# Optimization experiments

Hardware: AMD Instinct MI355X
Metric: run time of the kernel (lower is better)

The kernel has to match this reference:

```python
import jax, jax.numpy as jnp
import numpy as np

V, D, H, HD, T, B, L, BLK = 50257, 1024, 16, 64, 1024, 4, 6, 1024


def _ln_all(x):
    # F.layer_norm(x, (B, T, C)): normalize over the ENTIRE tensor, no affine
    mu = x.mean()
    var = ((x - mu) ** 2).mean()
    return (x - mu) * jax.lax.rsqrt(var + 1e-5)


def setup_inputs() -> dict:
    key = jax.random.key(0)
    ks = jax.random.split(key, 10)
    n = lambda k, shape, scale=1.0: jax.random.normal(k, shape, jnp.float32) * scale
    return {
        "idx": jax.random.randint(ks[0], (B, T), 0, V),
        "token_emb_table": n(ks[1], (V, D)),
        "position_emb_table": n(ks[2], (BLK, D)),
        "attention_q": n(ks[3], (D, H, HD), HD ** -0.5),
        "attention_k": n(ks[4], (D, H, HD), HD ** -0.5),
        "attention_v": n(ks[5], (D, H, HD), HD ** -0.5),
        "out_proj": n(ks[6], (H, HD, D), HD ** -0.5),
        "w_in": n(ks[7], (D, 4 * D), D ** -0.5),
        "w_out": n(ks[8], (4 * D, D), (4 * D) ** -0.5),
        "lm_head": n(ks[9], (D, V), D ** -0.5),
    }


def reference(idx, token_emb_table, position_emb_table, attention_q,
              attention_k, attention_v, out_proj, w_in, w_out, lm_head):
    Tt = idx.shape[1]
    x = token_emb_table[idx] + position_emb_table[:Tt]  # [B,T,D]
    mask = jnp.tril(jnp.ones((Tt, Tt), bool))
    scale = HD ** -0.5
    neg_inf = jnp.float32(-jnp.inf)
    # NOTE: the source shares ONE set of attention/MLP params across all layers.
    for _ in range(L):
        xn = _ln_all(x)
        q = jnp.einsum('btc,chd->bhtd', xn, attention_q)
        k = jnp.einsum('btc,chd->bhtd', xn, attention_k)
        v = jnp.einsum('btc,chd->bhtd', xn, attention_v)
        # verbatim (transposed-label) einsum from the source
        att = jnp.einsum('bhkd,bhqd->bhqk', q, k) * scale
        att = jnp.where(mask[None, None], att, neg_inf)
        att = jax.nn.softmax(att, axis=-1)
        out = jnp.einsum('bhqk,bhkd->bhqd', att, v)
        out = jnp.einsum('bhqd,hdc->bqc', out, out_proj)
        # dropout p=0 (eval) -> identity
        x = _ln_all(xn + out) + out
        # source bug: mlp_out = dropout(x) -> MLP (w_in/w_out) is dead code;
        # eval dropout is identity, so x = x + x
        x = x + x
    # forward returns x (post final full-tensor layernorm); lm_head unused w/o targets
    return _ln_all(x)
```

## Files before the change

### kernel.cpp

```cpp
#include <hip/hip_runtime.h>
#include <math.h>

#define TDIM 1024
#define DDIM 1024
#define NH   16
#define HDIM 64
#define BB   4
#define NLAYER 6
#define NTOK (BB*TDIM)
#define NELEM (NTOK*DDIM)

__global__ __launch_bounds__(256)
void k_embed(const int* __restrict__ idx, const float* __restrict__ tok,
             const float* __restrict__ pos, float* __restrict__ x) {
  int e4 = blockIdx.x * 256 + threadIdx.x;
  int e  = e4 * 4;
  int r  = e >> 10;
  int d  = e & 1023;
  int tp = r & (TDIM - 1);
  int id = idx[r];
  float4 a = *reinterpret_cast<const float4*>(&tok[(size_t)id * DDIM + d]);
  float4 p = *reinterpret_cast<const float4*>(&pos[(size_t)tp * DDIM + d]);
  float4 o = make_float4(a.x + p.x, a.y + p.y, a.z + p.z, a.w + p.w);
  reinterpret_cast<float4*>(x)[e4] = o;
}

__global__ __launch_bounds__(256)
void k_reduce1(const float* __restrict__ x, double* __restrict__ part) {
  int t = threadIdx.x;
  size_t base = (size_t)blockIdx.x * 1024;
  double s = 0.0, ss = 0.0;
  #pragma unroll
  for (int it = 0; it < 4; ++it) {
    double v = (double)x[base + it * 256 + t];
    s += v; ss += v * v;
  }
  __shared__ double rs[256], rq[256];
  rs[t] = s; rq[t] = ss; __syncthreads();
  for (int w = 128; w > 0; w >>= 1) {
    if (t < w) { rs[t] += rs[t + w]; rq[t] += rq[t + w]; }
    __syncthreads();
  }
  if (t == 0) { part[blockIdx.x * 2] = rs[0]; part[blockIdx.x * 2 + 1] = rq[0]; }
}

__global__ __launch_bounds__(1024)
void k_reduce2(const double* __restrict__ part, double* __restrict__ stats) {
  int t = threadIdx.x;
  double s = 0.0, ss = 0.0;
  #pragma unroll
  for (int it = 0; it < 4; ++it) {
    int p = it * 1024 + t;
    s  += part[p * 2];
    ss += part[p * 2 + 1];
  }
  __shared__ double rs[1024], rq[1024];
  rs[t] = s; rq[t] = ss; __syncthreads();
  for (int w = 512; w > 0; w >>= 1) {
    if (t < w) { rs[t] += rs[t + w]; rq[t] += rq[t + w]; }
    __syncthreads();
  }
  if (t == 0) {
    double mu  = rs[0] / (double)NELEM;
    double var = rq[0] / (double)NELEM - mu * mu;
    stats[0] = mu;
    stats[1] = 1.0 / sqrt(var + 1e-5);
  }
}

__global__ __launch_bounds__(256)
void k_norm4(const float* __restrict__ x, const double* __restrict__ stats,
             float* __restrict__ y) {
  int e4 = blockIdx.x * 256 + threadIdx.x;
  double mu = stats[0], rs = stats[1];
  float4 v = reinterpret_cast<const float4*>(x)[e4];
  float4 o = make_float4((float)(((double)v.x - mu) * rs),
                         (float)(((double)v.y - mu) * rs),
                         (float)(((double)v.z - mu) * rs),
                         (float)(((double)v.w - mu) * rs));
  reinterpret_cast<float4*>(y)[e4] = o;
}

__global__ __launch_bounds__(256)
void k_add4(float* __restrict__ t1, const float* __restrict__ proj) {
  int e4 = blockIdx.x * 256 + threadIdx.x;
  float4 a = reinterpret_cast<const float4*>(t1)[e4];
  float4 b = reinterpret_cast<const float4*>(proj)[e4];
  float4 o = make_float4(a.x + b.x, a.y + b.y, a.z + b.z, a.w + b.w);
  reinterpret_cast<float4*>(t1)[e4] = o;
}

__global__ __launch_bounds__(256)
void k_combine4(const float* __restrict__ t1, const float* __restrict__ proj,
                const double* __restrict__ stats, float* __restrict__ x) {
  int e4 = blockIdx.x * 256 + threadIdx.x;
  double mu = stats[0], rs = stats[1];
  float4 a = reinterpret_cast<const float4*>(t1)[e4];
  float4 b = reinterpret_cast<const float4*>(proj)[e4];
  float4 o = make_float4((float)(2.0 * (((double)a.x - mu) * rs + (double)b.x)),
                         (float)(2.0 * (((double)a.y - mu) * rs + (double)b.y)),
                         (float)(2.0 * (((double)a.z - mu) * rs + (double)b.z)),
                         (float)(2.0 * (((double)a.w - mu) * rs + (double)b.w)));
  reinterpret_cast<float4*>(x)[e4] = o;
}

__global__ __launch_bounds__(256)
void k_norm_out(const float* __restrict__ x, const double* __restrict__ stats,
                float* __restrict__ out) {
  int e4 = blockIdx.x * 256 + threadIdx.x;
  double mu = stats[0], rs = stats[1];
  float4 v = reinterpret_cast<const float4*>(x)[e4];
  float4 o = make_float4((float)(((double)v.x - mu) * rs),
                         (float)(((double)v.y - mu) * rs),
                         (float)(((double)v.z - mu) * rs),
                         (float)(((double)v.w - mu) * rs));
  reinterpret_cast<float4*>(out)[e4] = o;
}

__global__ __launch_bounds__(256)
void k_gemm(const float* __restrict__ A, const float* __restrict__ Bm,
            float* __restrict__ C, int scatter) {
  __shared__ float As[16][64];
  __shared__ float Bs[16][64];
  int t  = threadIdx.x;
  int m0 = blockIdx.y * 64;
  int n0 = blockIdx.x * 64;
  int tx = t & 15, ty = t >> 4;
  int ar = t >> 2;
  int ak = (t & 3) * 4;
  int br = t >> 4;
  int bc = (t & 15) * 4;
  double acc[4][4] = {};

  for (int kk = 0; kk < DDIM; kk += 16) {
    float4 av = *reinterpret_cast<const float4*>(&A[(size_t)(m0 + ar) * DDIM + kk + ak]);
    float4 bv = *reinterpret_cast<const float4*>(&Bm[(size_t)(kk + br) * DDIM + n0 + bc]);
    __syncthreads();
    As[ak + 0][ar] = av.x; As[ak + 1][ar] = av.y;
    As[ak + 2][ar] = av.z; As[ak + 3][ar] = av.w;
    Bs[br][bc + 0] = bv.x; Bs[br][bc + 1] = bv.y;
    Bs[br][bc + 2] = bv.z; Bs[br][bc + 3] = bv.w;
    __syncthreads();
    #pragma unroll
    for (int k = 0; k < 16; ++k) {
      float4 a4 = *reinterpret_cast<const float4*>(&As[k][ty * 4]);
      float4 b4 = *reinterpret_cast<const float4*>(&Bs[k][tx * 4]);
      double ad[4] = {(double)a4.x, (double)a4.y, (double)a4.z, (double)a4.w};
      double bd[4] = {(double)b4.x, (double)b4.y, (double)b4.z, (double)b4.w};
      #pragma unroll
      for (int i = 0; i < 4; ++i)
        #pragma unroll
        for (int j = 0; j < 4; ++j)
          acc[i][j] += ad[i] * bd[j];
    }
  }

  #pragma unroll
  for (int i = 0; i < 4; ++i) {
    int r  = m0 + ty * 4 + i;
    int b  = r >> 10;
    int tp = r & 1023;
    #pragma unroll
    for (int j = 0; j < 4; ++j) {
      int c = n0 + tx * 4 + j;
      float val = (float)acc[i][j];
      if (scatter) {
        int h = c >> 6, d = c & 63;
        C[((size_t)((b * NH + h) * TDIM + tp)) * HDIM + d] = val;
      } else {
        C[(size_t)r * DDIM + c] = val;
      }
    }
  }
}

__global__ __launch_bounds__(256)
void k_attn_flash(const float* __restrict__ q, const float* __restrict__ k,
                  const float* __restrict__ v, float* __restrict__ attout) {
  int it = blockIdx.x;
  int bh = blockIdx.y;
  int b  = bh >> 4, h = bh & 15;
  const float* qh = q + (size_t)bh * TDIM * HDIM;
  const float* kh = k + (size_t)bh * TDIM * HDIM;
  const float* vh = v + (size_t)bh * TDIM * HDIM;
  int i0 = it * 64;

  __shared__ float Ks[64][68];
  __shared__ float Qs[64][68];
  __shared__ float Vs[64][68];

  int t  = threadIdx.x;
  int tx = t & 15, ty = t >> 4;

  #pragma unroll
  for (int itr = 0; itr < 4; ++itr) {
    int f = t + 256 * itr;
    int r = f >> 4, dc = (f & 15) * 4;
    float4 val = *reinterpret_cast<const float4*>(&kh[(size_t)(i0 + r) * HDIM + dc]);
    Ks[dc + 0][r] = val.x; Ks[dc + 1][r] = val.y;
    Ks[dc + 2][r] = val.z; Ks[dc + 3][r] = val.w;
  }

  double O[4][4] = {};
  double m[4], l[4];
  #pragma unroll
  for (int i = 0; i < 4; ++i) { m[i] = -1.0e300; l[i] = 0.0; }

  for (int jt = 0; jt <= it; ++jt) {
    int j0 = jt * 64;

    float4 qv[4], vv[4];
    #pragma unroll
    for (int itr = 0; itr < 4; ++itr) {
      int f = t + 256 * itr;
      int r = f >> 4, dc = (f & 15) * 4;
      qv[itr] = *reinterpret_cast<const float4*>(&qh[(size_t)(j0 + r) * HDIM + dc]);
      vv[itr] = *reinterpret_cast<const float4*>(&vh[(size_t)(j0 + r) * HDIM + dc]);
    }
    __syncthreads();
    #pragma unroll
    for (int itr = 0; itr < 4; ++itr) {
      int f = t + 256 * itr;
      int r = f >> 4, dc = (f & 15) * 4;
      Qs[dc + 0][r] = qv[itr].x; Qs[dc + 1][r] = qv[itr].y;
      Qs[dc + 2][r] = qv[itr].z; Qs[dc + 3][r] = qv[itr].w;
      *reinterpret_cast<float4*>(&Vs[r][dc]) = vv[itr];
    }
    __syncthreads();

    double S[4][4] = {};
    #pragma unroll 16
    for (int d = 0; d < 64; ++d) {
      float4 kf = *reinterpret_cast<const float4*>(&Ks[d][ty * 4]);
      float4 qf = *reinterpret_cast<const float4*>(&Qs[d][tx * 4]);
      double kd[4] = {(double)kf.x, (double)kf.y, (double)kf.z, (double)kf.w};
      double qd[4] = {(double)qf.x, (double)qf.y, (double)qf.z, (double)qf.w};
      #pragma unroll
      for (int i = 0; i < 4; ++i)
        #pragma unroll
        for (int j = 0; j < 4; ++j)
          S[i][j] += kd[i] * qd[j];
    }

    double mloc[4];
    #pragma unroll
    for (int i = 0; i < 4; ++i) {
      #pragma unroll
      for (int j = 0; j < 4; ++j) {
        S[i][j] *= 0.125;
        if (jt == it && (tx * 4 + j) > (ty * 4 + i)) S[i][j] = -1.0e300;
      }
      mloc[i] = fmax(fmax(S[i][0], S[i][1]), fmax(S[i][2], S[i][3]));
    }
    #pragma unroll
    for (int xm = 1; xm < 16; xm <<= 1)
      #pragma unroll
      for (int i = 0; i < 4; ++i)
        mloc[i] = fmax(mloc[i], __shfl_xor(mloc[i], xm, 64));

    double p[4][4], tsum[4];
    #pragma unroll
    for (int i = 0; i < 4; ++i) {
      double mnew  = fmax(m[i], mloc[i]);
      double scale = exp(m[i] - mnew);
      m[i] = mnew;
      tsum[i] = 0.0;
      #pragma unroll
      for (int j = 0; j < 4; ++j) {
        p[i][j] = exp(S[i][j] - mnew);
        tsum[i] += p[i][j];
      }
      l[i] *= scale;
      #pragma unroll
      for (int j = 0; j < 4; ++j) O[i][j] *= scale;
    }
    #pragma unroll
    for (int xm = 1; xm < 16; xm <<= 1)
      #pragma unroll
      for (int i = 0; i < 4; ++i)
        tsum[i] += __shfl_xor(tsum[i], xm, 64);
    #pragma unroll
    for (int i = 0; i < 4; ++i) l[i] += tsum[i];

    __syncthreads();
    #pragma unroll
    for (int i = 0; i < 4; ++i)
      #pragma unroll
      for (int j = 0; j < 4; ++j)
        Qs[tx * 4 + j][ty * 4 + i] = (float)p[i][j];
    __syncthreads();

    #pragma unroll 16
    for (int jl = 0; jl < 64; ++jl) {
      float4 pf = *reinterpret_cast<const float4*>(&Qs[jl][ty * 4]);
      float4 vf = *reinterpret_cast<const float4*>(&Vs[jl][tx * 4]);
      double pd[4] = {(double)pf.x, (double)pf.y, (double)pf.z, (double)pf.w};
      double vd[4] = {(double)vf.x, (double)vf.y, (double)vf.z, (double)vf.w};
      #pragma unroll
      for (int i = 0; i < 4; ++i)
        #pragma unroll
        for (int j = 0; j < 4; ++j)
          O[i][j] += pd[i] * vd[j];
    }
  }

  #pragma unroll
  for (int i = 0; i < 4; ++i) {
    int ig = i0 + ty * 4 + i;
    double inv = 1.0 / l[i];
    float4 o;
    o.x = (float)(O[i][0] * inv); o.y = (float)(O[i][1] * inv);
    o.z = (float)(O[i][2] * inv); o.w = (float)(O[i][3] * inv);
    *reinterpret_cast<float4*>(
        &attout[((size_t)(b * TDIM + ig)) * DDIM + h * HDIM + tx * 4]) = o;
  }
}

extern "C" void kernel_launch(void* const* d_in, const int* in_sizes, int n_in,
                              void* d_out, int out_size, void* d_ws, size_t ws_size,
                              hipStream_t stream) {
  (void)in_sizes; (void)n_in; (void)out_size; (void)ws_size;
  const int*   idx = (const int*)d_in[0];
  const float* tok = (const float*)d_in[1];
  const float* pos = (const float*)d_in[2];
  const float* wq  = (const float*)d_in[3];
  const float* wk  = (const float*)d_in[4];
  const float* wv  = (const float*)d_in[5];
  const float* wo  = (const float*)d_in[6];
  float* out = (float*)d_out;

  float* ws   = (float*)d_ws;
  float* x    = ws;
  float* xn   = x   + NELEM;
  float* q    = xn  + NELEM;
  float* k    = q   + NELEM;
  float* v    = k   + NELEM;
  float* att  = x;
  float* proj = q;
  double* part  = (double*)(v + NELEM);
  double* stats = part + 8192;

  dim3 ggemm(DDIM / 64, NTOK / 64);
  dim3 gattn(TDIM / 64, BB * NH);

  k_embed<<<4096, 256, 0, stream>>>(idx, tok, pos, x);

  for (int l = 0; l < NLAYER; ++l) {
    k_reduce1<<<4096, 256, 0, stream>>>(x, part);
    k_reduce2<<<1, 1024, 0, stream>>>(part, stats);
    k_norm4<<<4096, 256, 0, stream>>>(x, stats, xn);
    k_gemm<<<ggemm, 256, 0, stream>>>(xn, wq, q, 1);
    k_gemm<<<ggemm, 256, 0, stream>>>(xn, wk, k, 1);
    k_gemm<<<ggemm, 256, 0, stream>>>(xn, wv, v, 1);
    k_attn_flash<<<gattn, 256, 0, stream>>>(q, k, v, att);
    k_gemm<<<ggemm, 256, 0, stream>>>(att, wo, proj, 0);
    k_add4<<<4096, 256, 0, stream>>>(xn, proj);
    k_reduce1<<<4096, 256, 0, stream>>>(xn, part);
    k_reduce2<<<1, 1024, 0, stream>>>(part, stats);
    k_combine4<<<4096, 256, 0, stream>>>(xn, proj, stats, x);
  }

  k_reduce1<<<4096, 256, 0, stream>>>(x, part);
  k_reduce2<<<1, 1024, 0, stream>>>(part, stats);
  k_norm_out<<<4096, 256, 0, stream>>>(x, stats, out);
}
```

Before: 9.107 ms.

## Store GEMM tiles as swizzled doubles with register prefetch; pair causal attention tiles

The GEMM now converts inputs to double once when writing shared memory, using padded and swizzled tiles. It prefetches the next global tile into registers while computing the current one, and writes outputs as float4. The attention kernel launches 8 blocks per head, each handling tile z and tile 15-z in turn, to balance causal work across blocks. This trades doubled shared memory and fewer, longer attention blocks for less per-FMA conversion and better load balance.

```diff
diff --git a/kernel.cpp b/kernel.cpp
--- a/kernel.cpp
+++ b/kernel.cpp
@@ -117,36 +117,49 @@
   reinterpret_cast<float4*>(out)[e4] = o;
 }
 
+#define SWZB(c) ((c) + ((c) >> 4))
 __global__ __launch_bounds__(256)
 void k_gemm(const float* __restrict__ A, const float* __restrict__ Bm,
             float* __restrict__ C, int scatter) {
-  __shared__ float As[16][64];
-  __shared__ float Bs[16][64];
+  __shared__ double As[16][68];
+  __shared__ double Bs[16][72];
   int t  = threadIdx.x;
   int m0 = blockIdx.y * 64;
   int n0 = blockIdx.x * 64;
   int tx = t & 15, ty = t >> 4;
-  int ar = t >> 2;
-  int ak = (t & 3) * 4;
-  int br = t >> 4;
-  int bc = (t & 15) * 4;
+  int ar = t >> 2, ak = (t & 3) * 4;
+  int br = t >> 4, bc = (t & 15) * 4;
+  int sb = SWZB(bc);
+
+  const float* Ap = &A[(size_t)(m0 + ar) * DDIM + ak];
+  const float* Bp = &Bm[(size_t)br * DDIM + n0 + bc];
+  float4 av = *reinterpret_cast<const float4*>(Ap);
+  float4 bv = *reinterpret_cast<const float4*>(Bp);
+
   double acc[4][4] = {};
+  int cA = ty * 4;
+  int cB = SWZB(tx * 4);
 
   for (int kk = 0; kk < DDIM; kk += 16) {
-    float4 av = *reinterpret_cast<const float4*>(&A[(size_t)(m0 + ar) * DDIM + kk + ak]);
-    float4 bv = *reinterpret_cast<const float4*>(&Bm[(size_t)(kk + br) * DDIM + n0 + bc]);
-    __syncthreads();
-    As[ak + 0][ar] = av.x; As[ak + 1][ar] = av.y;
-    As[ak + 2][ar] = av.z; As[ak + 3][ar] = av.w;
-    Bs[br][bc + 0] = bv.x; Bs[br][bc + 1] = bv.y;
-    Bs[br][bc + 2] = bv.z; Bs[br][bc + 3] = bv.w;
-    __syncthreads();
+    __syncthreads();
+    As[ak + 0][ar] = (double)av.x; As[ak + 1][ar] = (double)av.y;
+    As[ak + 2][ar] = (double)av.z; As[ak + 3][ar] = (double)av.w;
+    Bs[br][sb + 0] = (double)bv.x; Bs[br][sb + 1] = (double)bv.y;
+    Bs[br][sb + 2] = (double)bv.z; Bs[br][sb + 3] = (double)bv.w;
+    __syncthreads();
+
+    if (kk + 16 < DDIM) {
+      av = *reinterpret_cast<const float4*>(Ap + kk + 16);
+      bv = *reinterpret_cast<const float4*>(Bp + (size_t)(kk + 16) * DDIM);
+    }
+
     #pragma unroll
     for (int k = 0; k < 16; ++k) {
-      float4 a4 = *reinterpret_cast<const float4*>(&As[k][ty * 4]);
-      float4 b4 = *reinterpret_cast<const float4*>(&Bs[k][tx * 4]);
-      double ad[4] = {(double)a4.x, (double)a4.y, (double)a4.z, (double)a4.w};
-      double bd[4] = {(double)b4.x, (double)b4.y, (double)b4.z, (double)b4.w};
+      double ad[4], bd[4];
+      #pragma unroll
+      for (int i = 0; i < 4; ++i) ad[i] = As[k][cA + i];
+      #pragma unroll
+      for (int j = 0; j < 4; ++j) bd[j] = Bs[k][cB + j];
       #pragma unroll
       for (int i = 0; i < 4; ++i)
         #pragma unroll
@@ -160,16 +173,15 @@
     int r  = m0 + ty * 4 + i;
     int b  = r >> 10;
     int tp = r & 1023;
-    #pragma unroll
-    for (int j = 0; j < 4; ++j) {
-      int c = n0 + tx * 4 + j;
-      float val = (float)acc[i][j];
-      if (scatter) {
-        int h = c >> 6, d = c & 63;
-        C[((size_t)((b * NH + h) * TDIM + tp)) * HDIM + d] = val;
-      } else {
-        C[(size_t)r * DDIM + c] = val;
-      }
+    int cb = n0 + tx * 4;
+    float4 val = make_float4((float)acc[i][0], (float)acc[i][1],
+                             (float)acc[i][2], (float)acc[i][3]);
+    if (scatter) {
+      int h = cb >> 6, d = cb & 63;
+      *reinterpret_cast<float4*>(
+          &C[((size_t)((b * NH + h) * TDIM + tp)) * HDIM + d]) = val;
+    } else {
+      *reinterpret_cast<float4*>(&C[(size_t)r * DDIM + cb]) = val;
     }
   }
 }
@@ -177,13 +189,12 @@
 __global__ __launch_bounds__(256)
 void k_attn_flash(const float* __restrict__ q, const float* __restrict__ k,
                   const float* __restrict__ v, float* __restrict__ attout) {
-  int it = blockIdx.x;
+  int z  = blockIdx.x;
   int bh = blockIdx.y;
   int b  = bh >> 4, h = bh & 15;
   const float* qh = q + (size_t)bh * TDIM * HDIM;
   const float* kh = k + (size_t)bh * TDIM * HDIM;
   const float* vh = v + (size_t)bh * TDIM * HDIM;
-  int i0 = it * 64;
 
   __shared__ float Ks[64][68];
   __shared__ float Qs[64][68];
@@ -192,127 +203,134 @@
   int t  = threadIdx.x;
   int tx = t & 15, ty = t >> 4;
 
-  #pragma unroll
-  for (int itr = 0; itr < 4; ++itr) {
-    int f = t + 256 * itr;
-    int r = f >> 4, dc = (f & 15) * 4;
-    float4 val = *reinterpret_cast<const float4*>(&kh[(size_t)(i0 + r) * HDIM + dc]);
-    Ks[dc + 0][r] = val.x; Ks[dc + 1][r] = val.y;
-    Ks[dc + 2][r] = val.z; Ks[dc + 3][r] = val.w;
-  }
-
-  double O[4][4] = {};
-  double m[4], l[4];
-  #pragma unroll
-  for (int i = 0; i < 4; ++i) { m[i] = -1.0e300; l[i] = 0.0; }
-
-  for (int jt = 0; jt <= it; ++jt) {
-    int j0 = jt * 64;
-
-    float4 qv[4], vv[4];
+  for (int phase = 0; phase < 2; ++phase) {
+    int it = phase ? (15 - z) : z;
+    int i0 = it * 64;
+
+    __syncthreads();
+
     #pragma unroll
     for (int itr = 0; itr < 4; ++itr) {
       int f = t + 256 * itr;
       int r = f >> 4, dc = (f & 15) * 4;
-      qv[itr] = *reinterpret_cast<const float4*>(&qh[(size_t)(j0 + r) * HDIM + dc]);
-      vv[itr] = *reinterpret_cast<const float4*>(&vh[(size_t)(j0 + r) * HDIM + dc]);
-    }
-    __syncthreads();
+      float4 val = *reinterpret_cast<const float4*>(&kh[(size_t)(i0 + r) * HDIM + dc]);
+      Ks[dc + 0][r] = val.x; Ks[dc + 1][r] = val.y;
+      Ks[dc + 2][r] = val.z; Ks[dc + 3][r] = val.w;
+    }
+
+    double O[4][4] = {};
+    double m[4], l[4];
     #pragma unroll
-    for (int itr = 0; itr < 4; ++itr) {
-      int f = t + 256 * itr;
-      int r = f >> 4, dc = (f & 15) * 4;
-      Qs[dc + 0][r] = qv[itr].x; Qs[dc + 1][r] = qv[itr].y;
-      Qs[dc + 2][r] = qv[itr].z; Qs[dc + 3][r] = qv[itr].w;
-      *reinterpret_cast<float4*>(&Vs[r][dc]) = vv[itr];
-    }
-    __syncthreads();
-
-    double S[4][4] = {};
-    #pragma unroll 16
-    for (int d = 0; d < 64; ++d) {
-      float4 kf = *reinterpret_cast<const float4*>(&Ks[d][ty * 4]);
-      float4 qf = *reinterpret_cast<const float4*>(&Qs[d][tx * 4]);
-      double kd[4] = {(double)kf.x, (double)kf.y, (double)kf.z, (double)kf.w};
-      double qd[4] = {(double)qf.x, (double)qf.y, (double)qf.z, (double)qf.w};
+    for (int i = 0; i < 4; ++i) { m[i] = -1.0e300; l[i] = 0.0; }
+
+    for (int jt = 0; jt <= it; ++jt) {
+      int j0 = jt * 64;
+
+      float4 qv[4], vv[4];
+      #pragma unroll
+      for (int itr = 0; itr < 4; ++itr) {
+        int f = t + 256 * itr;
+        int r = f >> 4, dc = (f & 15) * 4;
+        qv[itr] = *reinterpret_cast<const float4*>(&qh[(size_t)(j0 + r) * HDIM + dc]);
+        vv[itr] = *reinterpret_cast<const float4*>(&vh[(size_t)(j0 + r) * HDIM + dc]);
+      }
+      __syncthreads();
+      #pragma unroll
+      for (int itr = 0; itr < 4; ++itr) {
+        int f = t + 256 * itr;
+        int r = f >> 4, dc = (f & 15) * 4;
+        Qs[dc + 0][r] = qv[itr].x; Qs[dc + 1][r] = qv[itr].y;
+        Qs[dc + 2][r] = qv[itr].z; Qs[dc + 3][r] = qv[itr].w;
+        *reinterpret_cast<float4*>(&Vs[r][dc]) = vv[itr];
+      }
+      __syncthreads();
+
+      double S[4][4] = {};
+      #pragma unroll 16
+      for (int d = 0; d < 64; ++d) {
+        float4 kf = *reinterpret_cast<const float4*>(&Ks[d][ty * 4]);
+        float4 qf = *reinterpret_cast<const float4*>(&Qs[d][tx * 4]);
+        double kd[4] = {(double)kf.x, (double)kf.y, (double)kf.z, (double)kf.w};
+        double qd[4] = {(double)qf.x, (double)qf.y, (double)qf.z, (double)qf.w};
+        #pragma unroll
+        for (int i = 0; i < 4; ++i)
+          #pragma unroll
+          for (int j = 0; j < 4; ++j)
+            S[i][j] += kd[i] * qd[j];
+      }
+
+      double mloc[4];
+      #pragma unroll
+      for (int i = 0; i < 4; ++i) {
+        #pragma unroll
+        for (int j = 0; j < 4; ++j) {
+          S[i][j] *= 0.125;
+          if (jt == it && (tx * 4 + j) > (ty * 4 + i)) S[i][j] = -1.0e300;
+        }
+        mloc[i] = fmax(fmax(S[i][0], S[i][1]), fmax(S[i][2], S[i][3]));
+      }
+      #pragma unroll
+      for (int xm = 1; xm < 16; xm <<= 1)
+        #pragma unroll
+        for (int i = 0; i < 4; ++i)
+          mloc[i] = fmax(mloc[i], __shfl_xor(mloc[i], xm, 64));
+
+      double p[4][4], tsum[4];
+      #pragma unroll
+      for (int i = 0; i < 4; ++i) {
+        double mnew  = fmax(m[i], mloc[i]);
+        double scale = exp(m[i] - mnew);
+        m[i] = mnew;
+        tsum[i] = 0.0;
+        #pragma unroll
+        for (int j = 0; j < 4; ++j) {
+          p[i][j] = exp(S[i][j] - mnew);
+          tsum[i] += p[i][j];
+        }
+        l[i] *= scale;
+        #pragma unroll
+        for (int j = 0; j < 4; ++j) O[i][j] *= scale;
+      }
+      #pragma unroll
+      for (int xm = 1; xm < 16; xm <<= 1)
+        #pragma unroll
+        for (int i = 0; i < 4; ++i)
+          tsum[i] += __shfl_xor(tsum[i], xm, 64);
+      #pragma unroll
+      for (int i = 0; i < 4; ++i) l[i] += tsum[i];
+
+      __syncthreads();
       #pragma unroll
       for (int i = 0; i < 4; ++i)
         #pragma unroll
         for (int j = 0; j < 4; ++j)
-          S[i][j] += kd[i] * qd[j];
-    }
-
-    double mloc[4];
+          Qs[tx * 4 + j][ty * 4 + i] = (float)p[i][j];
+      __syncthreads();
+
+      #pragma unroll 16
+      for (int jl = 0; jl < 64; ++jl) {
+        float4 pf = *reinterpret_cast<const float4*>(&Qs[jl][ty * 4]);
+        float4 vf = *reinterpret_cast<const float4*>(&Vs[jl][tx * 4]);
+        double pd[4] = {(double)pf.x, (double)pf.y, (double)pf.z, (double)pf.w};
+        double vd[4] = {(double)vf.x, (double)vf.y, (double)vf.z, (double)vf.w};
+        #pragma unroll
+        for (int i = 0; i < 4; ++i)
+          #pragma unroll
+          for (int j = 0; j < 4; ++j)
+            O[i][j] += pd[i] * vd[j];
+      }
+    }
+
     #pragma unroll
     for (int i = 0; i < 4; ++i) {
-      #pragma unroll
-      for (int j = 0; j < 4; ++j) {
-        S[i][j] *= 0.125;
-        if (jt == it && (tx * 4 + j) > (ty * 4 + i)) S[i][j] = -1.0e300;
-      }
-      mloc[i] = fmax(fmax(S[i][0], S[i][1]), fmax(S[i][2], S[i][3]));
-    }
-    #pragma unroll
-    for (int xm = 1; xm < 16; xm <<= 1)
-      #pragma unroll
-      for (int i = 0; i < 4; ++i)
-        mloc[i] = fmax(mloc[i], __shfl_xor(mloc[i], xm, 64));
-
-    double p[4][4], tsum[4];
-    #pragma unroll
-    for (int i = 0; i < 4; ++i) {
-      double mnew  = fmax(m[i], mloc[i]);
-      double scale = exp(m[i] - mnew);
-      m[i] = mnew;
-      tsum[i] = 0.0;
-      #pragma unroll
-      for (int j = 0; j < 4; ++j) {
-        p[i][j] = exp(S[i][j] - mnew);
-        tsum[i] += p[i][j];
-      }
-      l[i] *= scale;
-      #pragma unroll
-      for (int j = 0; j < 4; ++j) O[i][j] *= scale;
-    }
-    #pragma unroll
-    for (int xm = 1; xm < 16; xm <<= 1)
-      #pragma unroll
-      for (int i = 0; i < 4; ++i)
-        tsum[i] += __shfl_xor(tsum[i], xm, 64);
-    #pragma unroll
-    for (int i = 0; i < 4; ++i) l[i] += tsum[i];
-
-    __syncthreads();
-    #pragma unroll
-    for (int i = 0; i < 4; ++i)
-      #pragma unroll
-      for (int j = 0; j < 4; ++j)
-        Qs[tx * 4 + j][ty * 4 + i] = (float)p[i][j];
-    __syncthreads();
-
-    #pragma unroll 16
-    for (int jl = 0; jl < 64; ++jl) {
-      float4 pf = *reinterpret_cast<const float4*>(&Qs[jl][ty * 4]);
-      float4 vf = *reinterpret_cast<const float4*>(&Vs[jl][tx * 4]);
-      double pd[4] = {(double)pf.x, (double)pf.y, (double)pf.z, (double)pf.w};
-      double vd[4] = {(double)vf.x, (double)vf.y, (double)vf.z, (double)vf.w};
-      #pragma unroll
-      for (int i = 0; i < 4; ++i)
-        #pragma unroll
-        for (int j = 0; j < 4; ++j)
-          O[i][j] += pd[i] * vd[j];
-    }
-  }
-
-  #pragma unroll
-  for (int i = 0; i < 4; ++i) {
-    int ig = i0 + ty * 4 + i;
-    double inv = 1.0 / l[i];
-    float4 o;
-    o.x = (float)(O[i][0] * inv); o.y = (float)(O[i][1] * inv);
-    o.z = (float)(O[i][2] * inv); o.w = (float)(O[i][3] * inv);
-    *reinterpret_cast<float4*>(
-        &attout[((size_t)(b * TDIM + ig)) * DDIM + h * HDIM + tx * 4]) = o;
+      int ig = i0 + ty * 4 + i;
+      double inv = 1.0 / l[i];
+      float4 o;
+      o.x = (float)(O[i][0] * inv); o.y = (float)(O[i][1] * inv);
+      o.z = (float)(O[i][2] * inv); o.w = (float)(O[i][3] * inv);
+      *reinterpret_cast<float4*>(
+          &attout[((size_t)(b * TDIM + ig)) * DDIM + h * HDIM + tx * 4]) = o;
+    }
   }
 }
 
@@ -341,7 +359,7 @@
   double* stats = part + 8192;
 
   dim3 ggemm(DDIM / 64, NTOK / 64);
-  dim3 gattn(TDIM / 64, BB * NH);
+  dim3 gattn(8, BB * NH);
 
   k_embed<<<4096, 256, 0, stream>>>(idx, tok, pos, x);
 
```

After: 7.896 ms. -13.3%, faster.
